# Performance work log

Hardware: AMD Instinct MI355X
Metric: run time of the kernel (lower is better)

## Reference

```python
import jax, jax.numpy as jnp
import numpy as np

B, T, S = 4, 2048, 512
HID, ND, NH = 2048, 1024, 16
HD = HID // NH  # 128
GATING_INIT = -4.0


def setup_inputs() -> dict:
    key = jax.random.key(0)
    ks = jax.random.split(key, 12)
    sc_h = 1.0 / np.sqrt(HID)
    sc_n = 1.0 / np.sqrt(ND)
    mask = jax.random.bernoulli(ks[2], 0.9, (B, S))
    mask = mask.at[:, 0].set(True)  # avoid fully-masked rows (NaN softmax)
    return {
        "hidden_states": jax.random.normal(ks[0], (B, T, HID), jnp.float32),
        "notes": jax.random.normal(ks[1], (B, S, ND), jnp.float32),
        "notes_mask": mask,
        "q_w": jax.random.normal(ks[3], (HID, HID), jnp.float32) * sc_h,
        "q_b": jax.random.normal(ks[4], (HID,), jnp.float32) * 0.01,
        "k_w": jax.random.normal(ks[5], (HID, ND), jnp.float32) * sc_n,
        "k_b": jax.random.normal(ks[6], (HID,), jnp.float32) * 0.01,
        "v_w": jax.random.normal(ks[7], (HID, ND), jnp.float32) * sc_n,
        "v_b": jax.random.normal(ks[8], (HID,), jnp.float32) * 0.01,
        "o_w": jax.random.normal(ks[9], (HID, HID), jnp.float32) * sc_h,
        "o_b": jax.random.normal(ks[10], (HID,), jnp.float32) * 0.01,
        "gate": jnp.full((1,), GATING_INIT, jnp.float32),
    }


def reference(hidden_states, notes, notes_mask, q_w, q_b, k_w, k_b, v_w, v_b, o_w, o_b, gate):
    # projections (torch Linear: x @ W^T + b)
    q = hidden_states @ q_w.T + q_b            # (B,T,HID)
    k = notes @ k_w.T + k_b                    # (B,S,HID)
    v = notes @ v_w.T + v_b                    # (B,S,HID)
    q = q.reshape(B, T, NH, HD).transpose(0, 2, 1, 3)  # (B,H,T,D)
    k = k.reshape(B, S, NH, HD).transpose(0, 2, 1, 3)  # (B,H,S,D)
    v = v.reshape(B, S, NH, HD).transpose(0, 2, 1, 3)
    scores = jnp.einsum("bhtd,bhsd->bhts", q, k) / jnp.sqrt(jnp.float32(HD))
    scores = jnp.where(notes_mask[:, None, None, :], scores, -jnp.inf)
    attn = jax.nn.softmax(scores, axis=-1)
    context = jnp.einsum("bhts,bhsd->bhtd", attn, v)   # (B,H,T,D)
    g = jax.nn.sigmoid(gate).reshape(1, 1, 1, 1)
    context = (g * context).transpose(0, 2, 1, 3).reshape(B, T, HID)
    delta = context @ o_w.T + o_b
    return delta
```

## Files before the change

kernel.cpp:

```cpp
#include <hip/hip_runtime.h>
#include <hip/hip_bf16.h>
#include <stdint.h>

#define B_ 4
#define T_ 2048
#define S_ 512
#define HID_ 2048
#define ND_ 1024
#define NH_ 16
#define HD_ 128

typedef unsigned short u16;
typedef unsigned int u32;
typedef __attribute__((ext_vector_type(8))) short bf16x8;
typedef __attribute__((ext_vector_type(4))) float f32x4;
typedef __attribute__((ext_vector_type(16))) float f32x16;
typedef __attribute__((ext_vector_type(4))) float f4;
typedef __attribute__((ext_vector_type(4))) u16 us4;
typedef __attribute__((ext_vector_type(8))) u16 us8;
typedef __attribute__((ext_vector_type(4))) u32 u32x4;

__device__ inline u16 f2bf(float f) {
  unsigned u = __builtin_bit_cast(unsigned, f);
  u += 0x7FFFu + ((u >> 16) & 1u);
  return (u16)(u >> 16);
}

__device__ inline u32 cvtpk(float lo, float hi) {
  u32 r;
  asm("v_cvt_pk_bf16_f32 %0, %1, %2" : "=v"(r) : "v"(lo), "v"(hi));
  return r;
}

__device__ inline f32x4 mfma16(bf16x8 a, bf16x8 b, f32x4 c) {
  return __builtin_amdgcn_mfma_f32_16x16x32_bf16(a, b, c, 0, 0, 0);
}
__device__ inline f32x16 mfma32(bf16x8 a, bf16x8 b, f32x16 c) {
  return __builtin_amdgcn_mfma_f32_32x32x16_bf16(a, b, c, 0, 0, 0);
}

__device__ inline void gload_lds16(const u16* g, u16* l) {
  __builtin_amdgcn_global_load_lds(
      (const __attribute__((address_space(1))) unsigned int*)g,
      (__attribute__((address_space(3))) unsigned int*)l, 16, 0, 0);
}

__global__ __launch_bounds__(256) void convert_all(
    const float* __restrict__ h, const float* __restrict__ n,
    const float* __restrict__ qw, const float* __restrict__ kw,
    const float* __restrict__ vw, const float* __restrict__ ow,
    u16* __restrict__ dh, u16* __restrict__ dn, u16* __restrict__ dqw,
    u16* __restrict__ dkw, u16* __restrict__ dvw, u16* __restrict__ dow) {
  const int C0 = 4194304;
  const int C1 = C0 + 524288;
  const int C2 = C1 + 1048576;
  const int C3 = C2 + 524288;
  const int C4 = C3 + 524288;
  const int C5 = C4 + 1048576;
  for (int c = blockIdx.x * blockDim.x + threadIdx.x; c < C5;
       c += gridDim.x * blockDim.x) {
    const float* s; u16* d; int o;
    if (c < C0)      { s = h;  d = dh;  o = c; }
    else if (c < C1) { s = n;  d = dn;  o = c - C0; }
    else if (c < C2) { s = qw; d = dqw; o = c - C1; }
    else if (c < C3) { s = kw; d = dkw; o = c - C2; }
    else if (c < C4) { s = vw; d = dvw; o = c - C3; }
    else             { s = ow; d = dow; o = c - C4; }
    f4 v = ((const f4*)s)[o];
    us4 r = { f2bf(v[0]), f2bf(v[1]), f2bf(v[2]), f2bf(v[3]) };
    ((us4*)d)[o] = r;
  }
}

template <bool OUT_BF16>
__global__ __launch_bounds__(256) void gemm_bt(
    const u16* __restrict__ A, const u16* __restrict__ Bm,
    const float* __restrict__ bias, void* __restrict__ Cout,
    int M, int N, int K) {
  __shared__ u16 As[128 * 32];
  __shared__ u16 Bs[128 * 32];
  const int tid = threadIdx.x;
  const int lane = tid & 63;
  const int wave = tid >> 6;
  const int wr = (wave >> 1) * 64;
  const int wc = (wave & 1) * 64;
  const int c15 = lane & 15;
  const int g = lane >> 4;
  const int bx = blockIdx.x, by = blockIdx.y;

  const u16* gA = A + (size_t)(by * 128 + (tid >> 2)) * K + (tid & 3) * 8;
  const u16* gB = Bm + (size_t)(bx * 128 + (tid >> 2)) * K + (tid & 3) * 8;

  f32x4 acc[4][4];
#pragma unroll
  for (int i = 0; i < 4; ++i)
#pragma unroll
    for (int j = 0; j < 4; ++j) acc[i][j] = (f32x4){0.f, 0.f, 0.f, 0.f};

  for (int k0 = 0; k0 < K; k0 += 32) {
    gload_lds16(gA + k0, &As[wave * 512]);
    gload_lds16(gA + (size_t)64 * K + k0, &As[2048 + wave * 512]);
    gload_lds16(gB + k0, &Bs[wave * 512]);
    gload_lds16(gB + (size_t)64 * K + k0, &Bs[2048 + wave * 512]);
    __syncthreads();
    bf16x8 af[4], bfr[4];
#pragma unroll
    for (int mt = 0; mt < 4; ++mt)
      af[mt] = *(const bf16x8*)&As[(wr + mt * 16 + c15) * 32 + g * 8];
#pragma unroll
    for (int nt = 0; nt < 4; ++nt)
      bfr[nt] = *(const bf16x8*)&Bs[(wc + nt * 16 + c15) * 32 + g * 8];
#pragma unroll
    for (int mt = 0; mt < 4; ++mt)
#pragma unroll
      for (int nt = 0; nt < 4; ++nt)
        acc[mt][nt] = mfma16(af[mt], bfr[nt], acc[mt][nt]);
    __syncthreads();
  }

#pragma unroll
  for (int mt = 0; mt < 4; ++mt)
#pragma unroll
    for (int nt = 0; nt < 4; ++nt) {
      const int m = by * 128 + wr + mt * 16 + g * 4;
      const int n = bx * 128 + wc + nt * 16 + c15;
      const float bv = bias[n];
#pragma unroll
      for (int r = 0; r < 4; ++r) {
        const float v = acc[mt][nt][r] + bv;
        if (OUT_BF16)
          ((u16*)Cout)[(size_t)(m + r) * N + n] = f2bf(v);
        else
          ((float*)Cout)[(size_t)(m + r) * N + n] = v;
      }
    }
}

template <bool OUT_BF16>
__global__ __launch_bounds__(512, 2) void gemm8p(
    const u16* __restrict__ A, const u16* __restrict__ Bm,
    const float* __restrict__ bias, void* __restrict__ Cout,
    int M, int N, int K) {
  extern __shared__ u16 lds[];
  const int tid = threadIdx.x;
  const int lane = tid & 63, wave = tid >> 6;
  const int wm = wave >> 2, wn = wave & 3;
  const int c15 = lane & 15, g = lane >> 4;
  const int bid = blockIdx.y * gridDim.x + blockIdx.x;
  const int sw = (bid & 7) * 32 + (bid >> 3);
  const int bn = sw & 7, bm = sw >> 3;
  const int NT = K >> 6;

  const int r0 = wave * 8 + (lane >> 3);
  const int scol = ((lane & 7) * 16) ^ ((lane >> 5) << 5);
  const size_t dK = (size_t)64 * K;
  const u16* pAlo = A + (size_t)(bm * 256 + r0) * K + (scol >> 1);
  const u16* pAhi = A + (size_t)(bm * 256 + 128 + r0) * K + (scol >> 1);
  const u16* pBlo = Bm + (size_t)(bn * 256 + r0) * K + (scol >> 1);
  const u16* pBhi = Bm + (size_t)(bn * 256 + 128 + r0) * K + (scol >> 1);

#define STG(p, dst)                                  \
  do {                                               \
    gload_lds16((p), (dst) + wave * 512);            \
    gload_lds16((p) + dK, (dst) + 4096 + wave * 512);\
    (p) += 64;                                       \
  } while (0)

  const int sg = (g * 8) ^ ((c15 & 4) << 2);
  const int aoff = wm * 8192 + c15 * 64 + sg;
  const int boff = 16384 + (wn >> 1) * 8192 + (wn & 1) * 4096 + c15 * 64 + sg;

  f32x4 acc[8][4];
#pragma unroll
  for (int i = 0; i < 8; ++i)
#pragma unroll
    for (int j = 0; j < 4; ++j) acc[i][j] = (f32x4){0.f, 0.f, 0.f, 0.f};

  STG(pAlo, lds);
  STG(pAhi, lds + 8192);
  STG(pBlo, lds + 16384);
  STG(pBhi, lds + 24576);
  STG(pAlo, lds + 32768);
  STG(pAhi, lds + 40960);
  STG(pBlo, lds + 49152);
  STG(pBhi, lds + 57344);
  asm volatile("s_waitcnt vmcnt(8)" ::: "memory");
  __builtin_amdgcn_s_barrier();

  for (int j = 0; j < NT; ++j) {
    const int cu = (j & 1) << 15;
    const u16* cb = lds + cu;
    u16* rb = lds + cu;
    const bool s2 = (j + 2 < NT);

    bf16x8 aL[4][2], bL[2][2];
#pragma unroll
    for (int fm = 0; fm < 4; ++fm)
#pragma unroll
      for (int h = 0; h < 2; ++h)
        aL[fm][h] = *(const bf16x8*)(cb + aoff + fm * 1024 + h * 32);
#pragma unroll
    for (int fn = 0; fn < 2; ++fn)
#pragma unroll
      for (int h = 0; h < 2; ++h)
        bL[fn][h] = *(const bf16x8*)(cb + boff + fn * 1024 + h * 32);
    __builtin_amdgcn_s_barrier();
    asm volatile("s_waitcnt lgkmcnt(0)" ::: "memory");
    __builtin_amdgcn_sched_barrier(0);
    __builtin_amdgcn_s_setprio(1);
#pragma unroll
    for (int fm = 0; fm < 4; ++fm)
#pragma unroll
      for (int fn = 0; fn < 2; ++fn) {
        acc[fm][fn] = mfma16(aL[fm][0], bL[fn][0], acc[fm][fn]);
        acc[fm][fn] = mfma16(aL[fm][1], bL[fn][1], acc[fm][fn]);
      }
    __builtin_amdgcn_s_setprio(0);
    __builtin_amdgcn_s_barrier();

    bf16x8 bH[2][2];
#pragma unroll
    for (int fn = 0; fn < 2; ++fn)
#pragma unroll
      for (int h = 0; h < 2; ++h)
        bH[fn][h] = *(const bf16x8*)(cb + boff + (2 + fn) * 1024 + h * 32);
    __builtin_amdgcn_s_barrier();
    asm volatile("s_waitcnt lgkmcnt(0)" ::: "memory");
    __builtin_amdgcn_sched_barrier(0);
    __builtin_amdgcn_s_setprio(1);
#pragma unroll
    for (int fm = 0; fm < 4; ++fm)
#pragma unroll
      for (int fn = 0; fn < 2; ++fn) {
        acc[fm][2 + fn] = mfma16(aL[fm][0], bH[fn][0], acc[fm][2 + fn]);
        acc[fm][2 + fn] = mfma16(aL[fm][1], bH[fn][1], acc[fm][2 + fn]);
      }
    __builtin_amdgcn_s_setprio(0);
    __builtin_amdgcn_s_barrier();

    bf16x8 aH[4][2];
#pragma unroll
    for (int fm = 0; fm < 4; ++fm)
#pragma unroll
      for (int h = 0; h < 2; ++h)
        aH[fm][h] = *(const bf16x8*)(cb + aoff + (4 + fm) * 1024 + h * 32);
    if (s2) {
      STG(pBlo, rb + 16384);
      STG(pBhi, rb + 24576);
    }
    __builtin_amdgcn_s_barrier();
    asm volatile("s_waitcnt lgkmcnt(0)" ::: "memory");
    __builtin_amdgcn_sched_barrier(0);
    __builtin_amdgcn_s_setprio(1);
#pragma unroll
    for (int fm = 0; fm < 4; ++fm)
#pragma unroll
      for (int fn = 0; fn < 2; ++fn) {
        acc[4 + fm][2 + fn] = mfma16(aH[fm][0], bH[fn][0], acc[4 + fm][2 + fn]);
        acc[4 + fm][2 + fn] = mfma16(aH[fm][1], bH[fn][1], acc[4 + fm][2 + fn]);
      }
    __builtin_amdgcn_s_setprio(0);
    __builtin_amdgcn_s_barrier();

    if (s2) {
      STG(pAlo, rb);
      STG(pAhi, rb + 8192);
    }
    __builtin_amdgcn_s_setprio(1);
#pragma unroll
    for (int fm = 0; fm < 4; ++fm)
#pragma unroll
      for (int fn = 0; fn < 2; ++fn) {
        acc[4 + fm][fn] = mfma16(aH[fm][0], bL[fn][0], acc[4 + fm][fn]);
        acc[4 + fm][fn] = mfma16(aH[fm][1], bL[fn][1], acc[4 + fm][fn]);
      }
    __builtin_amdgcn_s_setprio(0);
    if (j + 1 < NT) {
      if (s2) asm volatile("s_waitcnt vmcnt(8)" ::: "memory");
      else    asm volatile("s_waitcnt vmcnt(0)" ::: "memory");
      __builtin_amdgcn_s_barrier();
    }
  }
#undef STG

#pragma unroll
  for (int mf = 0; mf < 8; ++mf)
#pragma unroll
    for (int nf = 0; nf < 4; ++nf) {
      const int m = bm * 256 + wm * 128 + mf * 16 + g * 4;
      const int n = bn * 256 + wn * 64 + nf * 16 + c15;
      const float bv = bias[n];
#pragma unroll
      for (int r = 0; r < 4; ++r) {
        const float v = acc[mf][nf][r] + bv;
        if (OUT_BF16)
          ((u16*)Cout)[(size_t)(m + r) * N + n] = f2bf(v);
        else
          ((float*)Cout)[(size_t)(m + r) * N + n] = v;
      }
    }
}

__global__ __launch_bounds__(256) void transpose_v(const u16* __restrict__ v,
                                                   u16* __restrict__ vt) {
  __shared__ u16 tile[32][36];
  const int s0 = blockIdx.x * 32;
  const int bh = blockIdx.y;
  const int d0 = blockIdx.z * 32;
  const int b = bh >> 4, h = bh & 15;
  const int tid = threadIdx.x;
  const int sl = tid >> 3, dl = (tid & 7) * 4;
  us4 val = *(const us4*)(v + (size_t)(b * S_ + s0 + sl) * HID_ + h * HD_ + d0 + dl);
  *(us4*)&tile[sl][dl] = val;
  __syncthreads();
  const int dl2 = tid >> 3, sl2 = (tid & 7) * 4;
  us4 outv = { tile[sl2 + 0][dl2], tile[sl2 + 1][dl2],
               tile[sl2 + 2][dl2], tile[sl2 + 3][dl2] };
  *(us4*)(vt + ((size_t)bh * HD_ + d0 + dl2) * S_ + s0 + sl2) = outv;
}

__global__ __launch_bounds__(256) void attn_fwd(
    const u16* __restrict__ q, const u16* __restrict__ k,
    const u16* __restrict__ vt, const int* __restrict__ mask,
    const float* __restrict__ gate, u16* __restrict__ ctx) {
  __shared__ u16 smem[17408];
  __shared__ float addend[S_];
  const int tid = threadIdx.x, lane = tid & 63, wave = tid >> 6;
  const int bh = blockIdx.y, b = bh >> 4, h = bh & 15;
  const int tw = blockIdx.x * 128 + wave * 32;
  const int l31 = lane & 31, hi = lane >> 5;

  const u16* kb  = k + (size_t)b * S_ * HID_ + h * HD_;
  const u16* vtb = vt + (size_t)bh * HD_ * S_;

  const u16* sp[4];
  int dj[4];
  u16* ldsbase;
  ptrdiff_t stride;
  if (wave < 2) {
    ldsbase = smem;
    stride = 32 * HID_;
#pragma unroll
    for (int i = 0; i < 4; ++i) {
      const int jj = wave * 4 + i;
      const int row = jj * 4 + (lane >> 4);
      const int cb = (lane & 15) * 16;
      const int cbp = cb ^ ((row & 7) << 4);
      sp[i] = kb + (size_t)row * HID_ + (cbp >> 1);
      dj[i] = jj * 512;
    }
  } else {
    ldsbase = smem + 8192;
    stride = 32;
#pragma unroll
    for (int i = 0; i < 4; ++i) {
      const int jj = (wave - 2) * 4 + i;
      const int d = jj * 16 + (lane >> 2);
      const int cb = (lane & 3) * 16;
      const int cbp = cb ^ ((d & 3) << 4);
      sp[i] = vtb + (size_t)d * S_ + (cbp >> 1);
      dj[i] = jj * 512;
    }
  }
#define STAGE(cur)                                            \
  do {                                                        \
    _Pragma("unroll") for (int i_ = 0; i_ < 4; ++i_) {        \
      gload_lds16(sp[i_], ldsbase + (cur) * 4096 + dj[i_]);   \
      sp[i_] += stride;                                       \
    }                                                         \
  } while (0)

  STAGE(0);

  for (int s = tid; s < S_; s += 256)
    addend[s] = mask[b * S_ + s] ? 0.f : -1e30f;

  const u16* qrow = q + (size_t)(b * T_ + tw + l31) * HID_ + h * HD_;
  bf16x8 qf[8];
#pragma unroll
  for (int dc = 0; dc < 8; ++dc)
    qf[dc] = *(const bf16x8*)&qrow[dc * 16 + hi * 8];

  int kofs[8];
#pragma unroll
  for (int dc = 0; dc < 8; ++dc)
    kofs[dc] = l31 * 128 + (((dc * 32 + hi * 16) ^ ((l31 & 7) << 4)) >> 1);
  const int vcol0 = ((hi * 16) ^ ((l31 & 3) << 4)) >> 1;
  const int vcol1 = ((32 + hi * 16) ^ ((l31 & 3) << 4)) >> 1;

  float m_run = -1e30f, l_run = 0.f;
  f32x16 ct[4];
#pragma unroll
  for (int i = 0; i < 4; ++i)
#pragma unroll
    for (int r = 0; r < 16; ++r) ct[i][r] = 0.f;
  const float scale = 0.08838834764831845f;

  __syncthreads();

  for (int it = 0; it < 16; ++it) {
    const int cur = it & 1;
    if (it < 15) STAGE(cur ^ 1);
    const int s0 = it * 32;
    const u16* kt = smem + cur * 4096;
    const u16* vl = smem + 8192 + cur * 4096;

    f32x16 st;
#pragma unroll
    for (int r = 0; r < 16; ++r) st[r] = 0.f;
    __builtin_amdgcn_s_setprio(1);
#pragma unroll
    for (int dc = 0; dc < 8; ++dc) {
      bf16x8 kf = *(const bf16x8*)&kt[kofs[dc]];
      st = mfma32(kf, qf[dc], st);
    }
    __builtin_amdgcn_s_setprio(0);

    float sc[16];
#pragma unroll
    for (int rq = 0; rq < 4; ++rq) {
      f4 ad = *(const f4*)&addend[s0 + rq * 8 + hi * 4];
#pragma unroll
      for (int m = 0; m < 4; ++m)
        sc[rq * 4 + m] = st[rq * 4 + m] * scale + ad[m];
    }
    float tm = sc[0];
#pragma unroll
    for (int i = 1; i < 16; ++i) tm = fmaxf(tm, sc[i]);
    tm = fmaxf(tm, __shfl_xor(tm, 32));
    const float nm = fmaxf(m_run, tm);
    if (!__all(nm - m_run <= 8.f)) {
      const float corr = __expf(m_run - nm);
      l_run *= corr;
#pragma unroll
      for (int db = 0; db < 4; ++db)
#pragma unroll
        for (int r = 0; r < 16; ++r) ct[db][r] *= corr;
      m_run = nm;
    }
    float p[16], ps = 0.f;
#pragma unroll
    for (int i = 0; i < 16; ++i) { p[i] = __expf(sc[i] - m_run); ps += p[i]; }
    ps += __shfl_xor(ps, 32);
    l_run += ps;

    u32 w[8], x[8];
#pragma unroll
    for (int q2 = 0; q2 < 4; ++q2) {
      w[2 * q2]     = cvtpk(p[4 * q2],     p[4 * q2 + 1]);
      w[2 * q2 + 1] = cvtpk(p[4 * q2 + 2], p[4 * q2 + 3]);
    }
#pragma unroll
    for (int i = 0; i < 8; ++i) x[i] = __shfl_xor((int)w[i], 32);
    const u32x4 f0 = hi ? (u32x4){x[2], x[3], w[2], w[3]}
                        : (u32x4){w[0], w[1], x[0], x[1]};
    const u32x4 f1 = hi ? (u32x4){x[6], x[7], w[6], w[7]}
                        : (u32x4){w[4], w[5], x[4], x[5]};
    const bf16x8 pf0 = __builtin_bit_cast(bf16x8, f0);
    const bf16x8 pf1 = __builtin_bit_cast(bf16x8, f1);

    __builtin_amdgcn_s_setprio(1);
#pragma unroll
    for (int db = 0; db < 4; ++db) {
      bf16x8 vf0 = *(const bf16x8*)&vl[db * 1024 + l31 * 32 + vcol0];
      ct[db] = mfma32(vf0, pf0, ct[db]);
      bf16x8 vf1 = *(const bf16x8*)&vl[db * 1024 + l31 * 32 + vcol1];
      ct[db] = mfma32(vf1, pf1, ct[db]);
    }
    __builtin_amdgcn_s_setprio(0);

    __syncthreads();
  }
#undef STAGE

  const float gsig = 1.f / (1.f + __expf(-gate[0]));
  const float inv = gsig / l_run;
  u16* c_lds = smem + wave * 4352;
#pragma unroll
  for (int db = 0; db < 4; ++db)
#pragma unroll
    for (int rq = 0; rq < 4; ++rq) {
      us4 o = { f2bf(ct[db][rq * 4 + 0] * inv), f2bf(ct[db][rq * 4 + 1] * inv),
                f2bf(ct[db][rq * 4 + 2] * inv), f2bf(ct[db][rq * 4 + 3] * inv) };
      *(us4*)&c_lds[l31 * 136 + db * 32 + rq * 8 + hi * 4] = o;
    }
  u16* crow = ctx + (size_t)(b * T_ + tw) * HID_ + h * HD_;
#pragma unroll
  for (int rep = 0; rep < 8; ++rep) {
    const int tt = (lane >> 4) + rep * 4;
    us8 valv = *(const us8*)&c_lds[tt * 136 + (lane & 15) * 8];
    *(us8*)&crow[(size_t)tt * HID_ + (lane & 15) * 8] = valv;
  }
}

extern "C" void kernel_launch(void* const* d_in, const int* in_sizes, int n_in,
                              void* d_out, int out_size, void* d_ws, size_t ws_size,
                              hipStream_t stream) {
  (void)in_sizes; (void)n_in; (void)out_size; (void)ws_size;
  const float* hs   = (const float*)d_in[0];
  const float* nts  = (const float*)d_in[1];
  const int*   mask = (const int*)d_in[2];
  const float* qw   = (const float*)d_in[3];
  const float* qb   = (const float*)d_in[4];
  const float* kw   = (const float*)d_in[5];
  const float* kbi  = (const float*)d_in[6];
  const float* vw   = (const float*)d_in[7];
  const float* vbi  = (const float*)d_in[8];
  const float* ow   = (const float*)d_in[9];
  const float* obi  = (const float*)d_in[10];
  const float* gate = (const float*)d_in[11];
  float* out = (float*)d_out;

  char* w = (char*)d_ws;
  u16* h_bf   = (u16*)(w + 0);
  u16* n_bf   = (u16*)(w + 33554432);
  u16* qw_bf  = (u16*)(w + 37748736);
  u16* kw_bf  = (u16*)(w + 46137344);
  u16* vw_bf  = (u16*)(w + 50331648);
  u16* ow_bf  = (u16*)(w + 54525952);
  u16* q_bf   = (u16*)(w + 62914560);
  u16* k_bf   = (u16*)(w + 96468992);
  u16* v_bf   = (u16*)(w + 104857600);
  u16* vt_bf  = (u16*)(w + 113246208);
  u16* ctx_bf = h_bf;

  hipFuncSetAttribute(reinterpret_cast<const void*>(&gemm8p<true>),
                      hipFuncAttributeMaxDynamicSharedMemorySize, 131072);
  hipFuncSetAttribute(reinterpret_cast<const void*>(&gemm8p<false>),
                      hipFuncAttributeMaxDynamicSharedMemorySize, 131072);

  convert_all<<<dim3(2048), dim3(256), 0, stream>>>(
      hs, nts, qw, kw, vw, ow, h_bf, n_bf, qw_bf, kw_bf, vw_bf, ow_bf);
  gemm_bt<true><<<dim3(16, 16), dim3(256), 0, stream>>>(
      n_bf, kw_bf, kbi, k_bf, 2048, 2048, 1024);
  gemm_bt<true><<<dim3(16, 16), dim3(256), 0, stream>>>(
      n_bf, vw_bf, vbi, v_bf, 2048, 2048, 1024);
  transpose_v<<<dim3(16, 64, 4), dim3(256), 0, stream>>>(v_bf, vt_bf);
  gemm8p<true><<<dim3(8, 32), dim3(512), 131072, stream>>>(
      h_bf, qw_bf, qb, q_bf, 8192, 2048, 2048);
  attn_fwd<<<dim3(16, 64), dim3(256), 0, stream>>>(
      q_bf, k_bf, vt_bf, mask, gate, ctx_bf);
  gemm8p<false><<<dim3(8, 32), dim3(512), 131072, stream>>>(
      ctx_bf, ow_bf, obi, out, 8192, 2048, 2048);
}
```

Before: 284.3 us.

## Merge K/V projections, reswizzle GEMM LDS, deepen attention K/V staging pipeline

The separate K and V projection launches become one launch whose z-dimension selects the weight, bias and output. The 8-wave GEMM switches to an XOR swizzle over eight row groups for its LDS writes and reads to cut bank conflicts, and its barriers become inline-asm s_barrier with a memory clobber. The attention kernel moves from a double-buffered to a four-slot K/V ring with a two-tile prefetch distance and partial vmcnt waits instead of full syncthreads. It also splits the QK dot product into two independent MFMA accumulator chains and changes the V tile swizzle. The ring doubles attention shared memory, which may reduce occupancy.

After: 258.8 us. 9.0% less time.

```diff
diff --git a/kernel.cpp b/kernel.cpp
--- a/kernel.cpp
+++ b/kernel.cpp
@@ -44,6 +44,8 @@
       (const __attribute__((address_space(1))) unsigned int*)g,
       (__attribute__((address_space(3))) unsigned int*)l, 16, 0, 0);
 }
+
+#define FENCED_BARRIER() asm volatile("s_barrier" ::: "memory")
 
 __global__ __launch_bounds__(256) void convert_all(
     const float* __restrict__ h, const float* __restrict__ n,
@@ -72,11 +74,16 @@
   }
 }
 
-template <bool OUT_BF16>
-__global__ __launch_bounds__(256) void gemm_bt(
-    const u16* __restrict__ A, const u16* __restrict__ Bm,
-    const float* __restrict__ bias, void* __restrict__ Cout,
-    int M, int N, int K) {
+__global__ __launch_bounds__(256) void gemm_kv(
+    const u16* __restrict__ A,
+    const u16* __restrict__ B0, const float* __restrict__ bias0,
+    u16* __restrict__ C0v,
+    const u16* __restrict__ B1, const float* __restrict__ bias1,
+    u16* __restrict__ C1v, int M, int N, int K) {
+  const u16* Bm = blockIdx.z ? B1 : B0;
+  const float* bias = blockIdx.z ? bias1 : bias0;
+  u16* Cout = blockIdx.z ? C1v : C0v;
+
   __shared__ u16 As[128 * 32];
   __shared__ u16 Bs[128 * 32];
   const int tid = threadIdx.x;
@@ -126,13 +133,8 @@
       const int n = bx * 128 + wc + nt * 16 + c15;
       const float bv = bias[n];
 #pragma unroll
-      for (int r = 0; r < 4; ++r) {
-        const float v = acc[mt][nt][r] + bv;
-        if (OUT_BF16)
-          ((u16*)Cout)[(size_t)(m + r) * N + n] = f2bf(v);
-        else
-          ((float*)Cout)[(size_t)(m + r) * N + n] = v;
-      }
+      for (int r = 0; r < 4; ++r)
+        Cout[(size_t)(m + r) * N + n] = f2bf(acc[mt][nt][r] + bv);
     }
 }
 
@@ -152,7 +154,7 @@
   const int NT = K >> 6;
 
   const int r0 = wave * 8 + (lane >> 3);
-  const int scol = ((lane & 7) * 16) ^ ((lane >> 5) << 5);
+  const int scol = ((lane & 7) * 16) ^ ((lane >> 3) << 4);
   const size_t dK = (size_t)64 * K;
   const u16* pAlo = A + (size_t)(bm * 256 + r0) * K + (scol >> 1);
   const u16* pAhi = A + (size_t)(bm * 256 + 128 + r0) * K + (scol >> 1);
@@ -166,9 +168,11 @@
     (p) += 64;                                       \
   } while (0)
 
-  const int sg = (g * 8) ^ ((c15 & 4) << 2);
-  const int aoff = wm * 8192 + c15 * 64 + sg;
-  const int boff = 16384 + (wn >> 1) * 8192 + (wn & 1) * 4096 + c15 * 64 + sg;
+  const int xsw = (c15 & 7) << 3;
+  const int colh0 = (g * 8) ^ xsw;
+  const int colh1 = (32 + g * 8) ^ xsw;
+  const int aoff = wm * 8192 + c15 * 64;
+  const int boff = 16384 + (wn >> 1) * 8192 + (wn & 1) * 4096 + c15 * 64;
 
   f32x4 acc[8][4];
 #pragma unroll
@@ -185,7 +189,7 @@
   STG(pBlo, lds + 49152);
   STG(pBhi, lds + 57344);
   asm volatile("s_waitcnt vmcnt(8)" ::: "memory");
-  __builtin_amdgcn_s_barrier();
+  FENCED_BARRIER();
 
   for (int j = 0; j < NT; ++j) {
     const int cu = (j & 1) << 15;
@@ -195,16 +199,16 @@
 
     bf16x8 aL[4][2], bL[2][2];
 #pragma unroll
-    for (int fm = 0; fm < 4; ++fm)
-#pragma unroll
-      for (int h = 0; h < 2; ++h)
-        aL[fm][h] = *(const bf16x8*)(cb + aoff + fm * 1024 + h * 32);
-#pragma unroll
-    for (int fn = 0; fn < 2; ++fn)
-#pragma unroll
-      for (int h = 0; h < 2; ++h)
-        bL[fn][h] = *(const bf16x8*)(cb + boff + fn * 1024 + h * 32);
-    __builtin_amdgcn_s_barrier();
+    for (int fm = 0; fm < 4; ++fm) {
+      aL[fm][0] = *(const bf16x8*)(cb + aoff + fm * 1024 + colh0);
+      aL[fm][1] = *(const bf16x8*)(cb + aoff + fm * 1024 + colh1);
+    }
+#pragma unroll
+    for (int fn = 0; fn < 2; ++fn) {
+      bL[fn][0] = *(const bf16x8*)(cb + boff + fn * 1024 + colh0);
+      bL[fn][1] = *(const bf16x8*)(cb + boff + fn * 1024 + colh1);
+    }
+    FENCED_BARRIER();
     asm volatile("s_waitcnt lgkmcnt(0)" ::: "memory");
     __builtin_amdgcn_sched_barrier(0);
     __builtin_amdgcn_s_setprio(1);
@@ -216,15 +220,15 @@
         acc[fm][fn] = mfma16(aL[fm][1], bL[fn][1], acc[fm][fn]);
       }
     __builtin_amdgcn_s_setprio(0);
-    __builtin_amdgcn_s_barrier();
+    FENCED_BARRIER();
 
     bf16x8 bH[2][2];
 #pragma unroll
-    for (int fn = 0; fn < 2; ++fn)
-#pragma unroll
-      for (int h = 0; h < 2; ++h)
-        bH[fn][h] = *(const bf16x8*)(cb + boff + (2 + fn) * 1024 + h * 32);
-    __builtin_amdgcn_s_barrier();
+    for (int fn = 0; fn < 2; ++fn) {
+      bH[fn][0] = *(const bf16x8*)(cb + boff + (2 + fn) * 1024 + colh0);
+      bH[fn][1] = *(const bf16x8*)(cb + boff + (2 + fn) * 1024 + colh1);
+    }
+    FENCED_BARRIER();
     asm volatile("s_waitcnt lgkmcnt(0)" ::: "memory");
     __builtin_amdgcn_sched_barrier(0);
     __builtin_amdgcn_s_setprio(1);
@@ -236,19 +240,19 @@
         acc[fm][2 + fn] = mfma16(aL[fm][1], bH[fn][1], acc[fm][2 + fn]);
       }
     __builtin_amdgcn_s_setprio(0);
-    __builtin_amdgcn_s_barrier();
+    FENCED_BARRIER();
 
     bf16x8 aH[4][2];
 #pragma unroll
-    for (int fm = 0; fm < 4; ++fm)
-#pragma unroll
-      for (int h = 0; h < 2; ++h)
-        aH[fm][h] = *(const bf16x8*)(cb + aoff + (4 + fm) * 1024 + h * 32);
+    for (int fm = 0; fm < 4; ++fm) {
+      aH[fm][0] = *(const bf16x8*)(cb + aoff + (4 + fm) * 1024 + colh0);
+      aH[fm][1] = *(const bf16x8*)(cb + aoff + (4 + fm) * 1024 + colh1);
+    }
     if (s2) {
       STG(pBlo, rb + 16384);
       STG(pBhi, rb + 24576);
     }
-    __builtin_amdgcn_s_barrier();
+    FENCED_BARRIER();
     asm volatile("s_waitcnt lgkmcnt(0)" ::: "memory");
     __builtin_amdgcn_sched_barrier(0);
     __builtin_amdgcn_s_setprio(1);
@@ -260,7 +264,7 @@
         acc[4 + fm][2 + fn] = mfma16(aH[fm][1], bH[fn][1], acc[4 + fm][2 + fn]);
       }
     __builtin_amdgcn_s_setprio(0);
-    __builtin_amdgcn_s_barrier();
+    FENCED_BARRIER();
 
     if (s2) {
       STG(pAlo, rb);
@@ -278,7 +282,7 @@
     if (j + 1 < NT) {
       if (s2) asm volatile("s_waitcnt vmcnt(8)" ::: "memory");
       else    asm volatile("s_waitcnt vmcnt(0)" ::: "memory");
-      __builtin_amdgcn_s_barrier();
+      FENCED_BARRIER();
     }
   }
 #undef STG
@@ -323,7 +327,7 @@
     const u16* __restrict__ q, const u16* __restrict__ k,
     const u16* __restrict__ vt, const int* __restrict__ mask,
     const float* __restrict__ gate, u16* __restrict__ ctx) {
-  __shared__ u16 smem[17408];
+  __shared__ u16 smem[32768];
   __shared__ float addend[S_];
   const int tid = threadIdx.x, lane = tid & 63, wave = tid >> 6;
   const int bh = blockIdx.y, b = bh >> 4, h = bh & 15;
@@ -350,14 +354,14 @@
       dj[i] = jj * 512;
     }
   } else {
-    ldsbase = smem + 8192;
+    ldsbase = smem + 16384;
     stride = 32;
 #pragma unroll
     for (int i = 0; i < 4; ++i) {
       const int jj = (wave - 2) * 4 + i;
       const int d = jj * 16 + (lane >> 2);
       const int cb = (lane & 3) * 16;
-      const int cbp = cb ^ ((d & 3) << 4);
+      const int cbp = cb ^ (((d >> 1) & 3) << 4);
       sp[i] = vtb + (size_t)d * S_ + (cbp >> 1);
       dj[i] = jj * 512;
     }
@@ -370,8 +374,6 @@
     }                                                         \
   } while (0)
 
-  STAGE(0);
-
   for (int s = tid; s < S_; s += 256)
     addend[s] = mask[b * S_ + s] ? 0.f : -1e30f;
 
@@ -381,12 +383,16 @@
   for (int dc = 0; dc < 8; ++dc)
     qf[dc] = *(const bf16x8*)&qrow[dc * 16 + hi * 8];
 
+  STAGE(0);
+  STAGE(1);
+
   int kofs[8];
 #pragma unroll
   for (int dc = 0; dc < 8; ++dc)
     kofs[dc] = l31 * 128 + (((dc * 32 + hi * 16) ^ ((l31 & 7) << 4)) >> 1);
-  const int vcol0 = ((hi * 16) ^ ((l31 & 3) << 4)) >> 1;
-  const int vcol1 = ((32 + hi * 16) ^ ((l31 & 3) << 4)) >> 1;
+  const int vswz = ((l31 >> 1) & 3) << 4;
+  const int vcol0 = ((hi * 16) ^ vswz) >> 1;
+  const int vcol1 = ((32 + hi * 16) ^ vswz) >> 1;
 
   float m_run = -1e30f, l_run = 0.f;
   f32x16 ct[4];
@@ -396,23 +402,26 @@
     for (int r = 0; r < 16; ++r) ct[i][r] = 0.f;
   const float scale = 0.08838834764831845f;
 
-  __syncthreads();
+  asm volatile("s_waitcnt vmcnt(4) lgkmcnt(0)" ::: "memory");
+  FENCED_BARRIER();
 
   for (int it = 0; it < 16; ++it) {
-    const int cur = it & 1;
-    if (it < 15) STAGE(cur ^ 1);
+    const int cur = it & 3;
+    if (it + 2 < 16) STAGE((it + 2) & 3);
     const int s0 = it * 32;
     const u16* kt = smem + cur * 4096;
-    const u16* vl = smem + 8192 + cur * 4096;
-
-    f32x16 st;
-#pragma unroll
-    for (int r = 0; r < 16; ++r) st[r] = 0.f;
+    const u16* vl = smem + 16384 + cur * 4096;
+
+    f32x16 st_a, st_b;
+#pragma unroll
+    for (int r = 0; r < 16; ++r) { st_a[r] = 0.f; st_b[r] = 0.f; }
     __builtin_amdgcn_s_setprio(1);
 #pragma unroll
-    for (int dc = 0; dc < 8; ++dc) {
-      bf16x8 kf = *(const bf16x8*)&kt[kofs[dc]];
-      st = mfma32(kf, qf[dc], st);
+    for (int dc = 0; dc < 4; ++dc) {
+      bf16x8 kf0 = *(const bf16x8*)&kt[kofs[dc]];
+      bf16x8 kf1 = *(const bf16x8*)&kt[kofs[4 + dc]];
+      st_a = mfma32(kf0, qf[dc], st_a);
+      st_b = mfma32(kf1, qf[4 + dc], st_b);
     }
     __builtin_amdgcn_s_setprio(0);
 
@@ -422,7 +431,7 @@
       f4 ad = *(const f4*)&addend[s0 + rq * 8 + hi * 4];
 #pragma unroll
       for (int m = 0; m < 4; ++m)
-        sc[rq * 4 + m] = st[rq * 4 + m] * scale + ad[m];
+        sc[rq * 4 + m] = (st_a[rq * 4 + m] + st_b[rq * 4 + m]) * scale + ad[m];
     }
     float tm = sc[0];
 #pragma unroll
@@ -469,9 +478,15 @@
     }
     __builtin_amdgcn_s_setprio(0);
 
-    __syncthreads();
+    if (it < 15) {
+      if (it < 14) asm volatile("s_waitcnt vmcnt(4)" ::: "memory");
+      else         asm volatile("s_waitcnt vmcnt(0)" ::: "memory");
+      FENCED_BARRIER();
+    }
   }
 #undef STAGE
+
+  __syncthreads();
 
   const float gsig = 1.f / (1.f + __expf(-gate[0]));
   const float inv = gsig / l_run;
@@ -531,10 +546,8 @@
 
   convert_all<<<dim3(2048), dim3(256), 0, stream>>>(
       hs, nts, qw, kw, vw, ow, h_bf, n_bf, qw_bf, kw_bf, vw_bf, ow_bf);
-  gemm_bt<true><<<dim3(16, 16), dim3(256), 0, stream>>>(
-      n_bf, kw_bf, kbi, k_bf, 2048, 2048, 1024);
-  gemm_bt<true><<<dim3(16, 16), dim3(256), 0, stream>>>(
-      n_bf, vw_bf, vbi, v_bf, 2048, 2048, 1024);
+  gemm_kv<<<dim3(16, 16, 2), dim3(256), 0, stream>>>(
+      n_bf, kw_bf, kbi, k_bf, vw_bf, vbi, v_bf, 2048, 2048, 1024);
   transpose_v<<<dim3(16, 64, 4), dim3(256), 0, stream>>>(v_bf, vt_bf);
   gemm8p<true><<<dim3(8, 32), dim3(512), 131072, stream>>>(
       h_bf, qw_bf, qb, q_bf, 8192, 2048, 2048);
```
